# Kernel tuning notes

Hardware: AMD Instinct MI355X
Metric: run time of the kernel (lower is better)

Reference implementation:

```python
import jax, jax.numpy as jnp
import numpy as np

WORD_LEN = 4094
MAX_LEN = 9
EMB = 512
HID = 256
BATCH = 32768


def setup_inputs() -> dict:
    key = jax.random.key(0)
    ks = jax.random.split(key, 16)
    s = 0.02
    return {
        "decode_word": jax.random.randint(ks[0], (BATCH, 1), 0, WORD_LEN),
        "hidden": jax.random.normal(ks[1], (BATCH, HID), jnp.float32),
        "encoder_output": jax.random.normal(ks[2], (BATCH, MAX_LEN, HID), jnp.float32),
        "emb_table": jax.random.normal(ks[3], (WORD_LEN, EMB), jnp.float32) * s,
        "atten_W": jax.random.normal(ks[4], (MAX_LEN, 2 * HID), jnp.float32) * s,
        "atten_b": jnp.zeros((MAX_LEN,), jnp.float32),
        "comb_W": jax.random.normal(ks[5], (EMB, EMB + HID), jnp.float32) * s,
        "comb_b": jnp.zeros((EMB,), jnp.float32),
        "W_ih": jax.random.normal(ks[6], (3 * HID, EMB), jnp.float32) * s,
        "b_ih": jnp.zeros((3 * HID,), jnp.float32),
        "W_hh": jax.random.normal(ks[7], (3 * HID, HID), jnp.float32) * s,
        "b_hh": jnp.zeros((3 * HID,), jnp.float32),
        "out_W": jax.random.normal(ks[8], (WORD_LEN, HID), jnp.float32) * s,
        "out_b": jnp.zeros((WORD_LEN,), jnp.float32),
    }


def reference(decode_word, hidden, encoder_output, emb_table, atten_W, atten_b,
              comb_W, comb_b, W_ih, b_ih, W_hh, b_hh, out_W, out_b):
    # embedding: [B,1,E]
    embedded = emb_table[decode_word]
    B = hidden.shape[0]
    # expand hidden to [B,L,H], concat with encoder_output -> attention scores [B,L,L]
    hx = jnp.broadcast_to(hidden[:, None, :], (B, MAX_LEN, HID))
    scores = jnp.einsum('blf,mf->blm', jnp.concatenate([encoder_output, hx], axis=2), atten_W) + atten_b
    atten_weight = jax.nn.softmax(scores, axis=2)
    # bmm: [B,L,L] @ [B,L,H] -> [B,L,H], then sum over L -> context [B,1,H]
    atten_applied = jnp.einsum('blm,bmh->blh', atten_weight, encoder_output)
    c_i = atten_applied.sum(axis=1)[:, None, :]
    # combine + relu: [B,1,E]
    x = jnp.concatenate([embedded, c_i], axis=2) @ comb_W.T + comb_b
    x = jax.nn.relu(x)[:, 0]  # [B,E]
    # GRUCell (PyTorch gate order: r, z, n)
    gi = x @ W_ih.T + b_ih
    gh = hidden @ W_hh.T + b_hh
    i_r, i_z, i_n = jnp.split(gi, 3, axis=1)
    h_r, h_z, h_n = jnp.split(gh, 3, axis=1)
    r = jax.nn.sigmoid(i_r + h_r)
    z = jax.nn.sigmoid(i_z + h_z)
    n = jnp.tanh(i_n + r * h_n)
    h_new = (1.0 - z) * n + z * hidden
    # output projection + log_softmax over vocab
    out = jax.nn.log_softmax(h_new @ out_W.T + out_b, axis=1)
    return out, h_new
```

## Files before the change

kernel.cpp:

```cpp
#include <hip/hip_runtime.h>

typedef __bf16 bf16x8 __attribute__((ext_vector_type(8)));
typedef float  f32x4  __attribute__((ext_vector_type(4)));

#define BATCH_ 32768
#define VOC 4094
#define LGT_STRIDE 8188

__device__ inline unsigned short f2bf(float f) {
    unsigned int u = __builtin_bit_cast(unsigned int, f);
    unsigned int r = u + 0x7FFFu + ((u >> 16) & 1u);
    return (unsigned short)(r >> 16);
}
__device__ inline float bf2f(unsigned short u) {
    unsigned int v = ((unsigned int)u) << 16;
    return __builtin_bit_cast(float, v);
}

__device__ inline f32x4 mfma16(bf16x8 a, bf16x8 b, f32x4 c) {
    return __builtin_amdgcn_mfma_f32_16x16x32_bf16(a, b, c, 0, 0, 0);
}

__global__ __launch_bounds__(256) void k_prep(
    const float* __restrict__ comb_W, const float* __restrict__ W_ih,
    const float* __restrict__ W_hh, const float* __restrict__ out_W,
    const float* __restrict__ b_ih, const float* __restrict__ b_hh,
    const float* __restrict__ out_b,
    unsigned short* __restrict__ cwb, unsigned short* __restrict__ wg2,
    unsigned short* __restrict__ owb, float* __restrict__ bg,
    float* __restrict__ obp) {
    int i = blockIdx.x * 256 + threadIdx.x;
    if (i < 512 * 768) cwb[i] = f2bf(comb_W[i]);
    if (i < 1024 * 768) {
        int row = i / 768, k = i - row * 768;
        int hgrp = row >> 6, g = (row >> 4) & 3, hl = row & 15;
        int h = hgrp * 16 + hl;
        float v;
        if (g == 0) v = (k < 512) ? W_ih[(size_t)h * 512 + k] : W_hh[(size_t)h * 256 + (k - 512)];
        else if (g == 1) v = (k < 512) ? W_ih[(size_t)(256 + h) * 512 + k] : W_hh[(size_t)(256 + h) * 256 + (k - 512)];
        else if (g == 2) v = (k < 512) ? W_ih[(size_t)(512 + h) * 512 + k] : 0.f;
        else v = (k < 512) ? 0.f : W_hh[(size_t)(512 + h) * 256 + (k - 512)];
        wg2[i] = f2bf(v);
    }
    if (i < 4096 * 256) {
        int r = i >> 8;
        owb[i] = (r < VOC) ? f2bf(out_W[i]) : (unsigned short)0;
    }
    if (i < 1024) {
        float v = (i < 512) ? (b_ih[i] + b_hh[i]) : ((i < 768) ? b_ih[i] : b_hh[i - 256]);
        bg[i] = v;
    }
    if (i < 4096) obp[i] = (i < VOC) ? out_b[i] : -1.0e30f;
}

__global__ __launch_bounds__(256) void k_attn(
    const int* __restrict__ dw, const float* __restrict__ hidden,
    const float* __restrict__ enc, const float* __restrict__ emb,
    const float* __restrict__ aW, const float* __restrict__ ab,
    unsigned short* __restrict__ xcat, unsigned short* __restrict__ xh) {
    __shared__ float sAW[9 * 516];
    __shared__ float sAB[9];
    int tid = threadIdx.x;
    for (int i = tid; i < 9 * 512; i += 256) {
        int m = i >> 9, k = i & 511;
        sAW[m * 516 + k] = aW[i];
    }
    if (tid < 9) sAB[tid] = ab[tid];
    __syncthreads();
    int w = tid >> 6, lane = tid & 63;
    int b = blockIdx.x * 4 + w;
    const float* encb = enc + (size_t)b * (9 * 256);
    float4 h4 = *(const float4*)(hidden + (size_t)b * 256 + 4 * lane);

    float4 e[9];
#pragma unroll
    for (int l = 0; l < 9; l++) e[l] = *(const float4*)(encb + l * 256 + 4 * lane);

    float u[9];
#pragma unroll
    for (int m = 0; m < 9; m++) {
        float4 a = *(const float4*)&sAW[m * 516 + 256 + 4 * lane];
        float v = h4.x * a.x + h4.y * a.y + h4.z * a.z + h4.w * a.w;
        v += __shfl_xor(v, 1);  v += __shfl_xor(v, 2);  v += __shfl_xor(v, 4);
        v += __shfl_xor(v, 8);  v += __shfl_xor(v, 16); v += __shfl_xor(v, 32);
        u[m] = v + sAB[m];
    }
    float wsum[9] = {0, 0, 0, 0, 0, 0, 0, 0, 0};
#pragma unroll
    for (int l = 0; l < 9; l++) {
        float p[9];
#pragma unroll
        for (int m = 0; m < 9; m++) {
            float4 a = *(const float4*)&sAW[m * 516 + 4 * lane];
            float v = e[l].x * a.x + e[l].y * a.y + e[l].z * a.z + e[l].w * a.w;
            v += __shfl_xor(v, 1);  v += __shfl_xor(v, 2);  v += __shfl_xor(v, 4);
            v += __shfl_xor(v, 8);  v += __shfl_xor(v, 16); v += __shfl_xor(v, 32);
            p[m] = v + u[m];
        }
        float mx = p[0];
#pragma unroll
        for (int m = 1; m < 9; m++) mx = fmaxf(mx, p[m]);
        float s = 0.f, ex[9];
#pragma unroll
        for (int m = 0; m < 9; m++) { ex[m] = __expf(p[m] - mx); s += ex[m]; }
        float inv = 1.f / s;
#pragma unroll
        for (int m = 0; m < 9; m++) wsum[m] += ex[m] * inv;
    }
    float c0 = 0, c1 = 0, c2 = 0, c3 = 0;
#pragma unroll
    for (int m = 0; m < 9; m++) {
        c0 += wsum[m] * e[m].x; c1 += wsum[m] * e[m].y;
        c2 += wsum[m] * e[m].z; c3 += wsum[m] * e[m].w;
    }
    ushort4 cb; cb.x = f2bf(c0); cb.y = f2bf(c1); cb.z = f2bf(c2); cb.w = f2bf(c3);
    *(ushort4*)(xcat + (size_t)b * 768 + 512 + 4 * lane) = cb;
    ushort4 hb; hb.x = f2bf(h4.x); hb.y = f2bf(h4.y); hb.z = f2bf(h4.z); hb.w = f2bf(h4.w);
    *(ushort4*)(xh + (size_t)b * 768 + 512 + 4 * lane) = hb;

    int word = dw[b];
    const float* er = emb + (size_t)word * 512 + 8 * lane;
    float4 e0 = *(const float4*)er;
    float4 e1 = *(const float4*)(er + 4);
    ushort4 w0; w0.x = f2bf(e0.x); w0.y = f2bf(e0.y); w0.z = f2bf(e0.z); w0.w = f2bf(e0.w);
    ushort4 w1; w1.x = f2bf(e1.x); w1.y = f2bf(e1.y); w1.z = f2bf(e1.z); w1.w = f2bf(e1.w);
    *(ushort4*)(xcat + (size_t)b * 768 + 8 * lane) = w0;
    *(ushort4*)(xcat + (size_t)b * 768 + 8 * lane + 4) = w1;
}

__global__ __launch_bounds__(512) void k_combine(
    const unsigned short* __restrict__ xcat, const unsigned short* __restrict__ cwb,
    const float* __restrict__ comb_b, unsigned short* __restrict__ xh) {
    __shared__ __align__(16) char smem[65536];
    int tid = threadIdx.x, w = tid >> 6, lane = tid & 63;
    int lo = lane & 15, hi = lane >> 4;
    int bm0 = blockIdx.x * 128, n0 = blockIdx.y * 128;
    const __bf16* A = (const __bf16*)xcat;
    const __bf16* Bw = (const __bf16*)cwb;
    f32x4 acc[8] = {};
    for (int kc = 0; kc < 3; kc++) {
        if (kc) __syncthreads();
#pragma unroll
        for (int it = 0; it < 8; it++) {
            int p = it * 8192 + tid * 16;
            int r = p >> 9, cg = (p >> 4) & 31;
            bf16x8 v = *(const bf16x8*)(Bw + (size_t)(n0 + r) * 768 + kc * 256 + cg * 8);
            *(bf16x8*)(smem + r * 512 + ((cg ^ (r & 7)) << 4)) = v;
        }
        bf16x8 Af[8];
#pragma unroll
        for (int ks = 0; ks < 8; ks++)
            Af[ks] = *(const bf16x8*)(A + (size_t)(bm0 + w * 16 + lo) * 768 + kc * 256 + ks * 32 + 8 * hi);
        __syncthreads();
#pragma unroll
        for (int ks = 0; ks < 8; ks++) {
#pragma unroll
            for (int nf = 0; nf < 8; nf++) {
                int row = nf * 16 + lo;
                bf16x8 bfr = *(const bf16x8*)(smem + row * 512 + (((ks * 4 + hi) ^ (lo & 7)) << 4));
                acc[nf] = mfma16(Af[ks], bfr, acc[nf]);
            }
        }
    }
#pragma unroll
    for (int nf = 0; nf < 8; nf++) {
        int col = n0 + nf * 16 + lo;
        float cb = comb_b[col];
#pragma unroll
        for (int r = 0; r < 4; r++) {
            int row = bm0 + w * 16 + hi * 4 + r;
            xh[(size_t)row * 768 + col] = f2bf(fmaxf(acc[nf][r] + cb, 0.f));
        }
    }
}

__global__ __launch_bounds__(512) void k_gru(
    const unsigned short* __restrict__ xh, const unsigned short* __restrict__ wg2,
    const float* __restrict__ bg, const float* __restrict__ hidden,
    float* __restrict__ hnew_out, unsigned short* __restrict__ hnb) {
    __shared__ __align__(16) char smem[65536];
    int tid = threadIdx.x, w = tid >> 6, lane = tid & 63;
    int lo = lane & 15, hi = lane >> 4;
    int bm0 = blockIdx.x * 128, n0 = blockIdx.y * 128;
    int h00 = blockIdx.y * 32;
    const __bf16* A = (const __bf16*)xh;
    const __bf16* Bw = (const __bf16*)wg2;
    f32x4 acc[8] = {};
    for (int kc = 0; kc < 3; kc++) {
        if (kc) __syncthreads();
#pragma unroll
        for (int it = 0; it < 8; it++) {
            int p = it * 8192 + tid * 16;
            int r = p >> 9, cg = (p >> 4) & 31;
            bf16x8 v = *(const bf16x8*)(Bw + (size_t)(n0 + r) * 768 + kc * 256 + cg * 8);
            *(bf16x8*)(smem + r * 512 + ((cg ^ (r & 7)) << 4)) = v;
        }
        bf16x8 Af[8];
#pragma unroll
        for (int ks = 0; ks < 8; ks++)
            Af[ks] = *(const bf16x8*)(A + (size_t)(bm0 + w * 16 + lo) * 768 + kc * 256 + ks * 32 + 8 * hi);
        __syncthreads();
#pragma unroll
        for (int ks = 0; ks < 8; ks++) {
#pragma unroll
            for (int nf = 0; nf < 8; nf++) {
                int row = nf * 16 + lo;
                bf16x8 bfr = *(const bf16x8*)(smem + row * 512 + (((ks * 4 + hi) ^ (lo & 7)) << 4));
                acc[nf] = mfma16(Af[ks], bfr, acc[nf]);
            }
        }
    }
#pragma unroll
    for (int hgrp = 0; hgrp < 2; hgrp++) {
        int col = h00 + hgrp * 16 + lo;
        float br = bg[col], bz = bg[256 + col], bi = bg[512 + col], bh = bg[768 + col];
#pragma unroll
        for (int r = 0; r < 4; r++) {
            int row = bm0 + w * 16 + hi * 4 + r;
            float rr = 1.f / (1.f + __expf(-(acc[hgrp * 4 + 0][r] + br)));
            float zz = 1.f / (1.f + __expf(-(acc[hgrp * 4 + 1][r] + bz)));
            float nn = tanhf(acc[hgrp * 4 + 2][r] + bi + rr * (acc[hgrp * 4 + 3][r] + bh));
            float hp = hidden[(size_t)row * 256 + col];
            float hn = zz * (hp - nn) + nn;
            hnew_out[(size_t)row * 256 + col] = hn;
            hnb[(size_t)row * 256 + col] = f2bf(hn);
        }
    }
}

__global__ __launch_bounds__(512) void k_logit(
    const unsigned short* __restrict__ hnb, const unsigned short* __restrict__ owb,
    const float* __restrict__ obp, unsigned short* __restrict__ lgt,
    float* __restrict__ psum) {
    __shared__ __align__(16) char smem[65536];
    int tid = threadIdx.x, w = tid >> 6, lane = tid & 63;
    int lo = lane & 15, hi = lane >> 4;
    int bm0 = blockIdx.x * 128, n0 = blockIdx.y * 128;

    const __bf16* Bw = (const __bf16*)owb;
#pragma unroll
    for (int it = 0; it < 8; it++) {
        int p = it * 8192 + tid * 16;
        int r = p >> 9, cg = (p >> 4) & 31;
        bf16x8 v = *(const bf16x8*)(Bw + (size_t)(n0 + r) * 256 + cg * 8);
        *(bf16x8*)(smem + r * 512 + ((cg ^ (r & 7)) << 4)) = v;
    }
    const __bf16* A = (const __bf16*)hnb;
    bf16x8 Af[8];
#pragma unroll
    for (int ks = 0; ks < 8; ks++)
        Af[ks] = *(const bf16x8*)(A + (size_t)(bm0 + w * 16 + lo) * 256 + ks * 32 + 8 * hi);
    __syncthreads();

    f32x4 acc[8] = {};
#pragma unroll
    for (int ks = 0; ks < 8; ks++) {
#pragma unroll
        for (int nf = 0; nf < 8; nf++) {
            int row = nf * 16 + lo;
            bf16x8 bfr = *(const bf16x8*)(smem + row * 512 + (((ks * 4 + hi) ^ (lo & 7)) << 4));
            acc[nf] = mfma16(Af[ks], bfr, acc[nf]);
        }
    }
    __syncthreads();

    unsigned short* T = (unsigned short*)smem;
    float se[4] = {0.f, 0.f, 0.f, 0.f};
#pragma unroll
    for (int nf = 0; nf < 8; nf++) {
        int col = n0 + nf * 16 + lo;
        float ob = obp[col];
#pragma unroll
        for (int r = 0; r < 4; r++) {
            float lg = acc[nf][r] + ob;
            se[r] += __expf(lg);
            T[(w * 16 + hi * 4 + r) * 136 + nf * 16 + lo] = f2bf(lg);
        }
    }
#pragma unroll
    for (int r = 0; r < 4; r++) {
        float v = se[r];
        v += __shfl_xor(v, 1); v += __shfl_xor(v, 2);
        v += __shfl_xor(v, 4); v += __shfl_xor(v, 8);
        se[r] = v;
    }
    if (lo == 0) {
#pragma unroll
        for (int r = 0; r < 4; r++)
            psum[(size_t)blockIdx.y * BATCH_ + bm0 + w * 16 + hi * 4 + r] = se[r];
    }
    __syncthreads();
#pragma unroll
    for (int it = 0; it < 4; it++) {
        int t = it * 512 + tid;
        int row = t >> 4, ch = t & 15;
        ushort4 a = *(ushort4*)(T + row * 136 + ch * 8);
        ushort4 b = *(ushort4*)(T + row * 136 + ch * 8 + 4);
        size_t base = (size_t)(bm0 + row) * LGT_STRIDE + n0 + ch * 8;
        *(ushort4*)(lgt + base) = a;
        *(ushort4*)(lgt + base + 4) = b;
    }
}

__global__ __launch_bounds__(256) void k_lse(
    const float* __restrict__ psum, float* __restrict__ lse) {
    int b = blockIdx.x * 256 + threadIdx.x;
    float t = 0.f;
#pragma unroll
    for (int s = 0; s < 32; s++) t += psum[(size_t)s * BATCH_ + b];
    lse[b] = __logf(t);
}

__global__ __launch_bounds__(256) void k_out2(
    const float* __restrict__ lse, float* __restrict__ out) {
    int b = blockIdx.x, tid = threadIdx.x;
    float l = lse[b];
    const unsigned short* rowp = (const unsigned short*)(out + (size_t)b * VOC);
    ushort4 a0 = *(const ushort4*)(rowp + tid * 8);
    ushort4 b0 = *(const ushort4*)(rowp + tid * 8 + 4);
    ushort4 a1 = *(const ushort4*)(rowp + 2048 + tid * 8);
    ushort4 b1 = *(const ushort4*)(rowp + 2048 + tid * 8 + 4);
    __syncthreads();
    float* orow = out + (size_t)b * VOC;
    int v0 = tid * 8;
    {
        float2 p;
        p.x = bf2f(a0.x) - l; p.y = bf2f(a0.y) - l; *(float2*)(orow + v0) = p;
        p.x = bf2f(a0.z) - l; p.y = bf2f(a0.w) - l; *(float2*)(orow + v0 + 2) = p;
        p.x = bf2f(b0.x) - l; p.y = bf2f(b0.y) - l; *(float2*)(orow + v0 + 4) = p;
        p.x = bf2f(b0.z) - l; p.y = bf2f(b0.w) - l; *(float2*)(orow + v0 + 6) = p;
    }
    int v1 = 2048 + tid * 8;
    {
        float2 p;
        p.x = bf2f(a1.x) - l; p.y = bf2f(a1.y) - l;
        if (v1 + 1 < VOC) *(float2*)(orow + v1) = p;
        p.x = bf2f(a1.z) - l; p.y = bf2f(a1.w) - l;
        if (v1 + 3 < VOC) *(float2*)(orow + v1 + 2) = p;
        p.x = bf2f(b1.x) - l; p.y = bf2f(b1.y) - l;
        if (v1 + 5 < VOC) *(float2*)(orow + v1 + 4) = p;
        p.x = bf2f(b1.z) - l; p.y = bf2f(b1.w) - l;
        if (v1 + 7 < VOC) *(float2*)(orow + v1 + 6) = p;
    }
}

extern "C" void kernel_launch(void* const* d_in, const int* in_sizes, int n_in,
                              void* d_out, int out_size, void* d_ws, size_t ws_size,
                              hipStream_t stream) {
    const int*   dw      = (const int*)d_in[0];
    const float* hidden  = (const float*)d_in[1];
    const float* enc     = (const float*)d_in[2];
    const float* emb     = (const float*)d_in[3];
    const float* aW      = (const float*)d_in[4];
    const float* ab      = (const float*)d_in[5];
    const float* comb_W  = (const float*)d_in[6];
    const float* comb_b  = (const float*)d_in[7];
    const float* W_ih    = (const float*)d_in[8];
    const float* b_ih    = (const float*)d_in[9];
    const float* W_hh    = (const float*)d_in[10];
    const float* b_hh    = (const float*)d_in[11];
    const float* out_W   = (const float*)d_in[12];
    const float* out_b   = (const float*)d_in[13];

    float* out = (float*)d_out;
    float* hnew_out = out + (size_t)BATCH_ * VOC;

    unsigned short* xcat = (unsigned short*)d_ws;
    unsigned short* xh   = xcat + (size_t)BATCH_ * 768;
    unsigned short* hnb  = xh + (size_t)BATCH_ * 768;
    float* psum          = (float*)(hnb + (size_t)BATCH_ * 256);
    float* lse           = psum + (size_t)32 * BATCH_;
    float* obp           = lse + BATCH_;
    unsigned short* cwb  = (unsigned short*)(obp + 4096);
    unsigned short* wg2  = cwb + 512 * 768;
    unsigned short* owb  = wg2 + 1024 * 768;
    float* bg            = (float*)(owb + 4096 * 256);

    k_prep<<<4096, 256, 0, stream>>>(comb_W, W_ih, W_hh, out_W, b_ih, b_hh, out_b,
                                     cwb, wg2, owb, bg, obp);
    k_attn<<<BATCH_ / 4, 256, 0, stream>>>(dw, hidden, enc, emb, aW, ab, xcat, xh);
    k_combine<<<dim3(BATCH_ / 128, 4), 512, 0, stream>>>(xcat, cwb, comb_b, xh);
    k_gru<<<dim3(BATCH_ / 128, 8), 512, 0, stream>>>(xh, wg2, bg, hidden, hnew_out, hnb);
    k_logit<<<dim3(BATCH_ / 128, 32), 512, 0, stream>>>(hnb, owb, obp,
                                                        (unsigned short*)out, psum);
    k_lse<<<BATCH_ / 256, 256, 0, stream>>>(psum, lse);
    k_out2<<<BATCH_, 256, 0, stream>>>(lse, out);
}
```

Before: 771.4 us.

## Use 4-wave blocks with 32-row warp tiles and XCD-aware block remapping

```diff
diff --git a/kernel.cpp b/kernel.cpp
--- a/kernel.cpp
+++ b/kernel.cpp
@@ -128,29 +128,34 @@
     *(ushort4*)(xcat + (size_t)b * 768 + 8 * lane + 4) = w1;
 }
 
-__global__ __launch_bounds__(512) void k_combine(
+__global__ __launch_bounds__(256, 2) void k_combine(
     const unsigned short* __restrict__ xcat, const unsigned short* __restrict__ cwb,
     const float* __restrict__ comb_b, unsigned short* __restrict__ xh) {
     __shared__ __align__(16) char smem[65536];
+    int wgid = blockIdx.x;
+    int xcd = wgid & 7, slot = wgid >> 3;
+    int bx = xcd * 32 + (slot & 31), by = slot >> 5;
     int tid = threadIdx.x, w = tid >> 6, lane = tid & 63;
     int lo = lane & 15, hi = lane >> 4;
-    int bm0 = blockIdx.x * 128, n0 = blockIdx.y * 128;
+    int bm0 = bx * 128, n0 = by * 128;
     const __bf16* A = (const __bf16*)xcat;
     const __bf16* Bw = (const __bf16*)cwb;
-    f32x4 acc[8] = {};
+    f32x4 acc[2][8] = {};
     for (int kc = 0; kc < 3; kc++) {
         if (kc) __syncthreads();
 #pragma unroll
-        for (int it = 0; it < 8; it++) {
-            int p = it * 8192 + tid * 16;
+        for (int it = 0; it < 16; it++) {
+            int p = it * 4096 + tid * 16;
             int r = p >> 9, cg = (p >> 4) & 31;
             bf16x8 v = *(const bf16x8*)(Bw + (size_t)(n0 + r) * 768 + kc * 256 + cg * 8);
             *(bf16x8*)(smem + r * 512 + ((cg ^ (r & 7)) << 4)) = v;
         }
-        bf16x8 Af[8];
-#pragma unroll
-        for (int ks = 0; ks < 8; ks++)
-            Af[ks] = *(const bf16x8*)(A + (size_t)(bm0 + w * 16 + lo) * 768 + kc * 256 + ks * 32 + 8 * hi);
+        bf16x8 Af[2][8];
+#pragma unroll
+        for (int mf = 0; mf < 2; mf++)
+#pragma unroll
+            for (int ks = 0; ks < 8; ks++)
+                Af[mf][ks] = *(const bf16x8*)(A + (size_t)(bm0 + w * 32 + mf * 16 + lo) * 768 + kc * 256 + ks * 32 + 8 * hi);
         __syncthreads();
 #pragma unroll
         for (int ks = 0; ks < 8; ks++) {
@@ -158,47 +163,55 @@
             for (int nf = 0; nf < 8; nf++) {
                 int row = nf * 16 + lo;
                 bf16x8 bfr = *(const bf16x8*)(smem + row * 512 + (((ks * 4 + hi) ^ (lo & 7)) << 4));
-                acc[nf] = mfma16(Af[ks], bfr, acc[nf]);
+                acc[0][nf] = mfma16(Af[0][ks], bfr, acc[0][nf]);
+                acc[1][nf] = mfma16(Af[1][ks], bfr, acc[1][nf]);
             }
         }
     }
 #pragma unroll
-    for (int nf = 0; nf < 8; nf++) {
-        int col = n0 + nf * 16 + lo;
-        float cb = comb_b[col];
-#pragma unroll
-        for (int r = 0; r < 4; r++) {
-            int row = bm0 + w * 16 + hi * 4 + r;
-            xh[(size_t)row * 768 + col] = f2bf(fmaxf(acc[nf][r] + cb, 0.f));
-        }
-    }
-}
-
-__global__ __launch_bounds__(512) void k_gru(
+    for (int mf = 0; mf < 2; mf++)
+#pragma unroll
+        for (int nf = 0; nf < 8; nf++) {
+            int col = n0 + nf * 16 + lo;
+            float cb = comb_b[col];
+#pragma unroll
+            for (int r = 0; r < 4; r++) {
+                int row = bm0 + w * 32 + mf * 16 + hi * 4 + r;
+                xh[(size_t)row * 768 + col] = f2bf(fmaxf(acc[mf][nf][r] + cb, 0.f));
+            }
+        }
+}
+
+__global__ __launch_bounds__(256, 2) void k_gru(
     const unsigned short* __restrict__ xh, const unsigned short* __restrict__ wg2,
     const float* __restrict__ bg, const float* __restrict__ hidden,
     float* __restrict__ hnew_out, unsigned short* __restrict__ hnb) {
     __shared__ __align__(16) char smem[65536];
+    int wgid = blockIdx.x;
+    int xcd = wgid & 7, slot = wgid >> 3;
+    int bx = xcd * 32 + (slot & 31), by = slot >> 5;
     int tid = threadIdx.x, w = tid >> 6, lane = tid & 63;
     int lo = lane & 15, hi = lane >> 4;
-    int bm0 = blockIdx.x * 128, n0 = blockIdx.y * 128;
-    int h00 = blockIdx.y * 32;
+    int bm0 = bx * 128, n0 = by * 128;
+    int h00 = by * 32;
     const __bf16* A = (const __bf16*)xh;
     const __bf16* Bw = (const __bf16*)wg2;
-    f32x4 acc[8] = {};
+    f32x4 acc[2][8] = {};
     for (int kc = 0; kc < 3; kc++) {
         if (kc) __syncthreads();
 #pragma unroll
-        for (int it = 0; it < 8; it++) {
-            int p = it * 8192 + tid * 16;
+        for (int it = 0; it < 16; it++) {
+            int p = it * 4096 + tid * 16;
             int r = p >> 9, cg = (p >> 4) & 31;
             bf16x8 v = *(const bf16x8*)(Bw + (size_t)(n0 + r) * 768 + kc * 256 + cg * 8);
             *(bf16x8*)(smem + r * 512 + ((cg ^ (r & 7)) << 4)) = v;
         }
-        bf16x8 Af[8];
-#pragma unroll
-        for (int ks = 0; ks < 8; ks++)
-            Af[ks] = *(const bf16x8*)(A + (size_t)(bm0 + w * 16 + lo) * 768 + kc * 256 + ks * 32 + 8 * hi);
+        bf16x8 Af[2][8];
+#pragma unroll
+        for (int mf = 0; mf < 2; mf++)
+#pragma unroll
+            for (int ks = 0; ks < 8; ks++)
+                Af[mf][ks] = *(const bf16x8*)(A + (size_t)(bm0 + w * 32 + mf * 16 + lo) * 768 + kc * 256 + ks * 32 + 8 * hi);
         __syncthreads();
 #pragma unroll
         for (int ks = 0; ks < 8; ks++) {
@@ -206,93 +219,108 @@
             for (int nf = 0; nf < 8; nf++) {
                 int row = nf * 16 + lo;
                 bf16x8 bfr = *(const bf16x8*)(smem + row * 512 + (((ks * 4 + hi) ^ (lo & 7)) << 4));
-                acc[nf] = mfma16(Af[ks], bfr, acc[nf]);
+                acc[0][nf] = mfma16(Af[0][ks], bfr, acc[0][nf]);
+                acc[1][nf] = mfma16(Af[1][ks], bfr, acc[1][nf]);
             }
         }
     }
 #pragma unroll
-    for (int hgrp = 0; hgrp < 2; hgrp++) {
-        int col = h00 + hgrp * 16 + lo;
-        float br = bg[col], bz = bg[256 + col], bi = bg[512 + col], bh = bg[768 + col];
-#pragma unroll
-        for (int r = 0; r < 4; r++) {
-            int row = bm0 + w * 16 + hi * 4 + r;
-            float rr = 1.f / (1.f + __expf(-(acc[hgrp * 4 + 0][r] + br)));
-            float zz = 1.f / (1.f + __expf(-(acc[hgrp * 4 + 1][r] + bz)));
-            float nn = tanhf(acc[hgrp * 4 + 2][r] + bi + rr * (acc[hgrp * 4 + 3][r] + bh));
-            float hp = hidden[(size_t)row * 256 + col];
-            float hn = zz * (hp - nn) + nn;
-            hnew_out[(size_t)row * 256 + col] = hn;
-            hnb[(size_t)row * 256 + col] = f2bf(hn);
-        }
-    }
-}
-
-__global__ __launch_bounds__(512) void k_logit(
+    for (int mf = 0; mf < 2; mf++)
+#pragma unroll
+        for (int hgrp = 0; hgrp < 2; hgrp++) {
+            int col = h00 + hgrp * 16 + lo;
+            float br = bg[col], bz = bg[256 + col], bi = bg[512 + col], bh = bg[768 + col];
+#pragma unroll
+            for (int r = 0; r < 4; r++) {
+                int row = bm0 + w * 32 + mf * 16 + hi * 4 + r;
+                float rr = 1.f / (1.f + __expf(-(acc[mf][hgrp * 4 + 0][r] + br)));
+                float zz = 1.f / (1.f + __expf(-(acc[mf][hgrp * 4 + 1][r] + bz)));
+                float nn = tanhf(acc[mf][hgrp * 4 + 2][r] + bi + rr * (acc[mf][hgrp * 4 + 3][r] + bh));
+                float hp = hidden[(size_t)row * 256 + col];
+                float hn = zz * (hp - nn) + nn;
+                hnew_out[(size_t)row * 256 + col] = hn;
+                hnb[(size_t)row * 256 + col] = f2bf(hn);
+            }
+        }
+}
+
+__global__ __launch_bounds__(256, 2) void k_logit(
     const unsigned short* __restrict__ hnb, const unsigned short* __restrict__ owb,
     const float* __restrict__ obp, unsigned short* __restrict__ lgt,
     float* __restrict__ psum) {
     __shared__ __align__(16) char smem[65536];
+    int wgid = blockIdx.x;
+    int xcd = wgid & 7, slot = wgid >> 3;
+    int bx = xcd * 32 + (slot & 31), by = slot >> 5;
     int tid = threadIdx.x, w = tid >> 6, lane = tid & 63;
     int lo = lane & 15, hi = lane >> 4;
-    int bm0 = blockIdx.x * 128, n0 = blockIdx.y * 128;
+    int bm0 = bx * 128, n0 = by * 128;
 
     const __bf16* Bw = (const __bf16*)owb;
 #pragma unroll
-    for (int it = 0; it < 8; it++) {
-        int p = it * 8192 + tid * 16;
+    for (int it = 0; it < 16; it++) {
+        int p = it * 4096 + tid * 16;
         int r = p >> 9, cg = (p >> 4) & 31;
         bf16x8 v = *(const bf16x8*)(Bw + (size_t)(n0 + r) * 256 + cg * 8);
         *(bf16x8*)(smem + r * 512 + ((cg ^ (r & 7)) << 4)) = v;
     }
     const __bf16* A = (const __bf16*)hnb;
-    bf16x8 Af[8];
-#pragma unroll
-    for (int ks = 0; ks < 8; ks++)
-        Af[ks] = *(const bf16x8*)(A + (size_t)(bm0 + w * 16 + lo) * 256 + ks * 32 + 8 * hi);
+    bf16x8 Af[2][8];
+#pragma unroll
+    for (int mf = 0; mf < 2; mf++)
+#pragma unroll
+        for (int ks = 0; ks < 8; ks++)
+            Af[mf][ks] = *(const bf16x8*)(A + (size_t)(bm0 + w * 32 + mf * 16 + lo) * 256 + ks * 32 + 8 * hi);
     __syncthreads();
 
-    f32x4 acc[8] = {};
+    f32x4 acc[2][8] = {};
 #pragma unroll
     for (int ks = 0; ks < 8; ks++) {
 #pragma unroll
         for (int nf = 0; nf < 8; nf++) {
             int row = nf * 16 + lo;
             bf16x8 bfr = *(const bf16x8*)(smem + row * 512 + (((ks * 4 + hi) ^ (lo & 7)) << 4));
-            acc[nf] = mfma16(Af[ks], bfr, acc[nf]);
+            acc[0][nf] = mfma16(Af[0][ks], bfr, acc[0][nf]);
+            acc[1][nf] = mfma16(Af[1][ks], bfr, acc[1][nf]);
         }
     }
     __syncthreads();
 
     unsigned short* T = (unsigned short*)smem;
-    float se[4] = {0.f, 0.f, 0.f, 0.f};
-#pragma unroll
-    for (int nf = 0; nf < 8; nf++) {
-        int col = n0 + nf * 16 + lo;
-        float ob = obp[col];
+    float se[2][4] = {};
+#pragma unroll
+    for (int mf = 0; mf < 2; mf++)
+#pragma unroll
+        for (int nf = 0; nf < 8; nf++) {
+            int col = n0 + nf * 16 + lo;
+            float ob = obp[col];
+#pragma unroll
+            for (int r = 0; r < 4; r++) {
+                float lg = acc[mf][nf][r] + ob;
+                se[mf][r] += __expf(lg);
+                T[(w * 32 + mf * 16 + hi * 4 + r) * 136 + nf * 16 + lo] = f2bf(lg);
+            }
+        }
+#pragma unroll
+    for (int mf = 0; mf < 2; mf++)
 #pragma unroll
         for (int r = 0; r < 4; r++) {
-            float lg = acc[nf][r] + ob;
-            se[r] += __expf(lg);
-            T[(w * 16 + hi * 4 + r) * 136 + nf * 16 + lo] = f2bf(lg);
-        }
-    }
-#pragma unroll
-    for (int r = 0; r < 4; r++) {
-        float v = se[r];
-        v += __shfl_xor(v, 1); v += __shfl_xor(v, 2);
-        v += __shfl_xor(v, 4); v += __shfl_xor(v, 8);
-        se[r] = v;
-    }
+            float v = se[mf][r];
+            v += __shfl_xor(v, 1); v += __shfl_xor(v, 2);
+            v += __shfl_xor(v, 4); v += __shfl_xor(v, 8);
+            se[mf][r] = v;
+        }
     if (lo == 0) {
 #pragma unroll
-        for (int r = 0; r < 4; r++)
-            psum[(size_t)blockIdx.y * BATCH_ + bm0 + w * 16 + hi * 4 + r] = se[r];
+        for (int mf = 0; mf < 2; mf++)
+#pragma unroll
+            for (int r = 0; r < 4; r++)
+                psum[(size_t)by * BATCH_ + bm0 + w * 32 + mf * 16 + hi * 4 + r] = se[mf][r];
     }
     __syncthreads();
 #pragma unroll
-    for (int it = 0; it < 4; it++) {
-        int t = it * 512 + tid;
+    for (int it = 0; it < 8; it++) {
+        int t = it * 256 + tid;
         int row = t >> 4, ch = t & 15;
         ushort4 a = *(ushort4*)(T + row * 136 + ch * 8);
         ushort4 b = *(ushort4*)(T + row * 136 + ch * 8 + 4);
@@ -379,10 +407,9 @@
     k_prep<<<4096, 256, 0, stream>>>(comb_W, W_ih, W_hh, out_W, b_ih, b_hh, out_b,
                                      cwb, wg2, owb, bg, obp);
     k_attn<<<BATCH_ / 4, 256, 0, stream>>>(dw, hidden, enc, emb, aW, ab, xcat, xh);
-    k_combine<<<dim3(BATCH_ / 128, 4), 512, 0, stream>>>(xcat, cwb, comb_b, xh);
-    k_gru<<<dim3(BATCH_ / 128, 8), 512, 0, stream>>>(xh, wg2, bg, hidden, hnew_out, hnb);
-    k_logit<<<dim3(BATCH_ / 128, 32), 512, 0, stream>>>(hnb, owb, obp,
-                                                        (unsigned short*)out, psum);
+    k_combine<<<1024, 256, 0, stream>>>(xcat, cwb, comb_b, xh);
+    k_gru<<<2048, 256, 0, stream>>>(xh, wg2, bg, hidden, hnew_out, hnb);
+    k_logit<<<8192, 256, 0, stream>>>(hnb, owb, obp, (unsigned short*)out, psum);
     k_lse<<<BATCH_ / 256, 256, 0, stream>>>(psum, lse);
     k_out2<<<BATCH_, 256, 0, stream>>>(lse, out);
 }
```

Result: no change. 774.0 us (+0.3%).
